# Kernel tuning notes

Measured on AMD Instinct MI355X. Metric: run time of the kernel, lower is better.

## Reference

```python
import jax, jax.numpy as jnp
import numpy as np

D_MODEL = 1024
N_HEADS = 16
HEAD_DIM = D_MODEL // N_HEADS


def setup_inputs() -> dict:
    key = jax.random.key(0)
    k_x, k_qkv, k_out = jax.random.split(key, 3)
    B, T = 4, 2048
    x = jax.random.normal(k_x, (B, T, D_MODEL), dtype=jnp.float32)
    # Linear(bias=False): y = x @ W, with W stored as [in, out]
    W_qkv = jax.random.normal(k_qkv, (D_MODEL, 3 * D_MODEL), dtype=jnp.float32) * (D_MODEL ** -0.5)
    W_out = jax.random.normal(k_out, (D_MODEL, D_MODEL), dtype=jnp.float32) * (D_MODEL ** -0.5)
    return {"x": x, "W_qkv": W_qkv, "W_out": W_out}


def reference(x, W_qkv, W_out):
    B, T, C = x.shape
    H, Dh = N_HEADS, HEAD_DIM
    scale = 1.0 / jnp.sqrt(jnp.asarray(Dh, dtype=x.dtype))

    qkv = x @ W_qkv  # [B,T,3C]
    q, k, v = jnp.split(qkv, 3, axis=-1)

    def split_heads(t):
        return t.reshape(B, T, H, Dh).transpose(0, 2, 1, 3)  # [B,H,T,Dh]

    q, k, v = split_heads(q), split_heads(k), split_heads(v)

    scores = jnp.einsum('bhqd,bhkd->bhqk', q, k) * scale  # [B,H,T,T]
    causal = jnp.tril(jnp.ones((T, T), dtype=bool))
    scores = jnp.where(causal, scores, jnp.asarray(-jnp.inf, dtype=scores.dtype))
    attn = jax.nn.softmax(scores, axis=-1)
    # dropout p=0.0 -> identity
    out = jnp.einsum('bhqk,bhkd->bhqd', attn, v)  # [B,H,T,Dh]
    out = out.transpose(0, 2, 1, 3).reshape(B, T, C)
    return out @ W_out
```

## Files before the change

### kernel.cpp

```cpp
#include <hip/hip_runtime.h>
#include <stdint.h>

typedef unsigned short u16;
typedef float f32x4 __attribute__((ext_vector_type(4)));
typedef short s16x8 __attribute__((ext_vector_type(8)));

#define SEQ 2048
#define DM 1024
#define NH 16
#define HD 64
#define BATCH 4
#define ROWS (BATCH*SEQ)
#define QTILES (SEQ/64)

__device__ __forceinline__ u16 f32_bf16(float f) {
  union { float f; uint32_t u; } c; c.f = f;
  uint32_t u = c.u;
  return (u16)((u + 0x7fffu + ((u >> 16) & 1u)) >> 16);
}
__device__ __forceinline__ u16 f32_bf16_trunc(float f) {
  union { float f; uint32_t u; } c; c.f = f;
  return (u16)(c.u >> 16);
}

#define GLOAD_LDS16(g, l) __builtin_amdgcn_global_load_lds( \
    (__attribute__((address_space(1))) void*)(g),           \
    (__attribute__((address_space(3))) void*)(l), 16, 0, 0)

__global__ __launch_bounds__(256) void cast_bf16_k(const float* __restrict__ in,
                                                   u16* __restrict__ out, int n4) {
  int i = blockIdx.x * 256 + threadIdx.x;
  if (i >= n4) return;
  float4 v = ((const float4*)in)[i];
  ushort4 o;
  o.x = f32_bf16(v.x); o.y = f32_bf16(v.y); o.z = f32_bf16(v.z); o.w = f32_bf16(v.w);
  ((ushort4*)out)[i] = o;
}

__global__ __launch_bounds__(256) void cast_transpose_k(const float* __restrict__ in,
                                                        u16* __restrict__ out, int R, int C) {
  __shared__ float tile[32][33];
  int c0 = blockIdx.x * 32, r0 = blockIdx.y * 32;
  int t = threadIdx.x;
  int lr = t >> 3, lc = (t & 7) * 4;
  float4 v = *(const float4*)(in + (size_t)(r0 + lr) * C + c0 + lc);
  tile[lr][lc] = v.x; tile[lr][lc + 1] = v.y; tile[lr][lc + 2] = v.z; tile[lr][lc + 3] = v.w;
  __syncthreads();
  ushort4 o;
  o.x = f32_bf16(tile[lc + 0][lr]);
  o.y = f32_bf16(tile[lc + 1][lr]);
  o.z = f32_bf16(tile[lc + 2][lr]);
  o.w = f32_bf16(tile[lc + 3][lr]);
  *(ushort4*)(out + (size_t)(c0 + lr) * R + r0 + lc) = o;
}

#define QSCALE 0.18033688011112042f


__device__ __forceinline__ f32x4 mfma16(s16x8 a, s16x8 b, f32x4 c) {
  return __builtin_amdgcn_mfma_f32_16x16x32_bf16(a, b, c, 0, 0, 0);
}

template<int STG, int ENDVM, int LAST>
__device__ __forceinline__ void tile_step(
    const u16* lAc, const u16* lBc,
    const u16* lAn, const u16* lBn,
    u16* lAs, u16* lBs,
    const u16* gA0, const u16* gA1, const u16* gB0, const u16* gB1,
    int d0, int d1, int aoff, int boff,
    s16x8 (&fa)[4], s16x8 (&fb)[4],
    s16x8 (&na)[4], s16x8 (&nb)[4],
    f32x4 (&acc)[8][4])
{
  __builtin_amdgcn_s_barrier();
  __builtin_amdgcn_sched_barrier(0);
  s16x8 f1[4];
#pragma unroll
  for (int mi = 0; mi < 4; ++mi) f1[mi] = *(const s16x8*)&lAc[aoff + 2048 + mi * 512];
  if (STG) { GLOAD_LDS16(gA0, lAs + d0); GLOAD_LDS16(gA1, lAs + d1); }
  asm volatile("s_waitcnt lgkmcnt(4)" ::: "memory");
  __builtin_amdgcn_sched_barrier(0);
  __builtin_amdgcn_s_setprio(1);
#pragma unroll
  for (int mi = 0; mi < 4; ++mi)
#pragma unroll
    for (int ni = 0; ni < 4; ++ni)
      acc[mi][ni] = mfma16(fa[mi], fb[ni], acc[mi][ni]);
  __builtin_amdgcn_s_setprio(0);
  __builtin_amdgcn_sched_barrier(0);
  if (STG) { GLOAD_LDS16(gB0, lBs + d0); GLOAD_LDS16(gB1, lBs + d1); }
  if (ENDVM == 8)      asm volatile("s_waitcnt vmcnt(8)" ::: "memory");
  else if (ENDVM == 4) asm volatile("s_waitcnt vmcnt(4)" ::: "memory");
  else if (ENDVM == 0) asm volatile("s_waitcnt vmcnt(0)" ::: "memory");
  __builtin_amdgcn_s_barrier();
  __builtin_amdgcn_sched_barrier(0);
  if (!LAST) {
#pragma unroll
    for (int ni = 0; ni < 4; ++ni) nb[ni] = *(const s16x8*)&lBn[boff + ni * 512];
#pragma unroll
    for (int mi = 0; mi < 4; ++mi) na[mi] = *(const s16x8*)&lAn[aoff + mi * 512];
    asm volatile("s_waitcnt lgkmcnt(8)" ::: "memory");
  } else {
    asm volatile("s_waitcnt lgkmcnt(0)" ::: "memory");
  }
  __builtin_amdgcn_sched_barrier(0);
  __builtin_amdgcn_s_setprio(1);
#pragma unroll
  for (int mi = 0; mi < 4; ++mi)
#pragma unroll
    for (int ni = 0; ni < 4; ++ni)
      acc[4 + mi][ni] = mfma16(f1[mi], fb[ni], acc[4 + mi][ni]);
  __builtin_amdgcn_s_setprio(0);
  __builtin_amdgcn_sched_barrier(0);
}

__global__ __launch_bounds__(512, 2) void qkv_gemm(
    const u16* __restrict__ A, const u16* __restrict__ Bt,
    u16* __restrict__ Qo, u16* __restrict__ Ko, u16* __restrict__ Vo)
{
  __shared__ u16 lA[4][8192];
  __shared__ u16 lB[4][8192];
  int t = threadIdx.x;

  int flat = blockIdx.y * 12 + blockIdx.x;
  int swz = (flat & 7) * 48 + (flat >> 3);
  int by = swz / 12, bx = swz - by * 12;
  int m0 = by * 256, n0 = bx * 256;

  int lane = t & 63, w = t >> 6;
  int m16 = lane & 15, quad = lane >> 4;
  int wm = w >> 2, wn = w & 3;

  int r0 = t >> 2;
  int scol = ((t & 3) ^ ((t >> 3) & 3)) * 8;
  const u16* Ag0 = A  + (size_t)(m0 + r0) * DM + scol;
  const u16* Ag1 = A  + (size_t)(m0 + 128 + r0) * DM + scol;
  const u16* Bg0 = Bt + (size_t)(n0 + r0) * DM + scol;
  const u16* Bg1 = Bt + (size_t)(n0 + 128 + r0) * DM + scol;
  int d0 = t * 8, d1 = 4096 + t * 8;

  int ka = (quad ^ ((m16 >> 1) & 3)) * 8;
  int aoff = (wm * 128 + m16) * 32 + ka;
  int boff = (wn * 64 + m16) * 32 + ka;

  f32x4 acc[8][4];
#pragma unroll
  for (int mi = 0; mi < 8; ++mi)
#pragma unroll
    for (int ni = 0; ni < 4; ++ni)
#pragma unroll
      for (int r = 0; r < 4; ++r) acc[mi][ni][r] = 0.f;

#pragma unroll
  for (int kt = 0; kt < 3; ++kt) {
    GLOAD_LDS16(Ag0 + kt * 32, lA[kt] + d0);
    GLOAD_LDS16(Ag1 + kt * 32, lA[kt] + d1);
    GLOAD_LDS16(Bg0 + kt * 32, lB[kt] + d0);
    GLOAD_LDS16(Bg1 + kt * 32, lB[kt] + d1);
  }
  asm volatile("s_waitcnt vmcnt(8)" ::: "memory");
  __builtin_amdgcn_s_barrier();
  __builtin_amdgcn_sched_barrier(0);

  s16x8 fa0[4], fb0[4], fa1[4], fb1[4];
#pragma unroll
  for (int ni = 0; ni < 4; ++ni) fb0[ni] = *(const s16x8*)&lB[0][boff + ni * 512];
#pragma unroll
  for (int mi = 0; mi < 4; ++mi) fa0[mi] = *(const s16x8*)&lA[0][aoff + mi * 512];

  for (int it = 0; it < 14; ++it) {
    int T = 2 * it;
    tile_step<1, 8, 0>(lA[T & 3], lB[T & 3], lA[(T + 1) & 3], lB[(T + 1) & 3],
                       lA[(T + 3) & 3], lB[(T + 3) & 3],
                       Ag0 + (T + 3) * 32, Ag1 + (T + 3) * 32,
                       Bg0 + (T + 3) * 32, Bg1 + (T + 3) * 32,
                       d0, d1, aoff, boff, fa0, fb0, fa1, fb1, acc);
    tile_step<1, 8, 0>(lA[(T + 1) & 3], lB[(T + 1) & 3], lA[(T + 2) & 3], lB[(T + 2) & 3],
                       lA[(T + 4) & 3], lB[(T + 4) & 3],
                       Ag0 + (T + 4) * 32, Ag1 + (T + 4) * 32,
                       Bg0 + (T + 4) * 32, Bg1 + (T + 4) * 32,
                       d0, d1, aoff, boff, fa1, fb1, fa0, fb0, acc);
  }
  tile_step<1, 8, 0>(lA[0], lB[0], lA[1], lB[1], lA[3], lB[3],
                     Ag0 + 31 * 32, Ag1 + 31 * 32, Bg0 + 31 * 32, Bg1 + 31 * 32,
                     d0, d1, aoff, boff, fa0, fb0, fa1, fb1, acc);
  tile_step<0, 4, 0>(lA[1], lB[1], lA[2], lB[2], lA[0], lB[0],
                     Ag0, Ag1, Bg0, Bg1, d0, d1, aoff, boff, fa1, fb1, fa0, fb0, acc);
  tile_step<0, 0, 0>(lA[2], lB[2], lA[3], lB[3], lA[0], lB[0],
                     Ag0, Ag1, Bg0, Bg1, d0, d1, aoff, boff, fa0, fb0, fa1, fb1, acc);
  tile_step<0, -1, 1>(lA[3], lB[3], lA[0], lB[0], lA[0], lB[0],
                      Ag0, Ag1, Bg0, Bg1, d0, d1, aoff, boff, fa1, fb1, fa0, fb0, acc);

#pragma unroll
  for (int mi = 0; mi < 8; ++mi) {
    int gr = m0 + wm * 128 + mi * 16 + quad * 4;
    int b = gr >> 11, tt = gr & 2047;
#pragma unroll
    for (int ni = 0; ni < 4; ++ni) {
      int gc = n0 + wn * 64 + ni * 16 + m16;
      int sec = gc >> 10, rem = gc & 1023, h = rem >> 6, d = rem & 63;
      if (sec == 0) {
#pragma unroll
        for (int r = 0; r < 4; ++r)
          Qo[(((size_t)b * NH + h) * SEQ + tt + r) * HD + d] = f32_bf16(acc[mi][ni][r] * QSCALE);
      } else if (sec == 1) {
#pragma unroll
        for (int r = 0; r < 4; ++r)
          Ko[(((size_t)b * NH + h) * SEQ + tt + r) * HD + d] = f32_bf16(acc[mi][ni][r]);
      } else {
        ushort4 o;
        o.x = f32_bf16(acc[mi][ni][0]); o.y = f32_bf16(acc[mi][ni][1]);
        o.z = f32_bf16(acc[mi][ni][2]); o.w = f32_bf16(acc[mi][ni][3]);
        *(ushort4*)&Vo[(((size_t)b * NH + h) * HD + d) * SEQ + tt] = o;
      }
    }
  }
}

template<int EPI>
__global__ __launch_bounds__(256) void gemm_bt(
    const u16* __restrict__ A, const u16* __restrict__ Bt,
    float* __restrict__ Cf, u16* __restrict__ Qo, u16* __restrict__ Ko, u16* __restrict__ Vo,
    int M, int N, int K)
{
  __shared__ u16 As[128 * 32];
  __shared__ u16 Bs[128 * 32];
  int t = threadIdx.x;
  int m0 = blockIdx.y * 128, n0 = blockIdx.x * 128;

  int srow = t >> 2, scol8 = (t & 3) * 8;
  const u16* Ag0 = A  + (size_t)(m0 + srow) * K + scol8;
  const u16* Ag1 = A  + (size_t)(m0 + 64 + srow) * K + scol8;
  const u16* Bg0 = Bt + (size_t)(n0 + srow) * K + scol8;
  const u16* Bg1 = Bt + (size_t)(n0 + 64 + srow) * K + scol8;
  u16* Al0 = As + t * 8;  u16* Al1 = As + 2048 + t * 8;
  u16* Bl0 = Bs + t * 8;  u16* Bl1 = Bs + 2048 + t * 8;

  int lane = t & 63, w = t >> 6;
  int m16 = lane & 15, quad = lane >> 4;
  int wr = (w >> 1) * 64, wc = (w & 1) * 64;

  f32x4 acc[4][4];
#pragma unroll
  for (int mi = 0; mi < 4; ++mi)
#pragma unroll
    for (int ni = 0; ni < 4; ++ni)
#pragma unroll
      for (int r = 0; r < 4; ++r) acc[mi][ni][r] = 0.f;

  for (int k0 = 0; k0 < K; k0 += 32) {
    __syncthreads();
    GLOAD_LDS16(Ag0 + k0, Al0);
    GLOAD_LDS16(Ag1 + k0, Al1);
    GLOAD_LDS16(Bg0 + k0, Bl0);
    GLOAD_LDS16(Bg1 + k0, Bl1);
    __syncthreads();
    s16x8 af[4], bf[4];
#pragma unroll
    for (int mi = 0; mi < 4; ++mi)
      af[mi] = *(const s16x8*)(As + (wr + mi * 16 + m16) * 32 + quad * 8);
#pragma unroll
    for (int ni = 0; ni < 4; ++ni)
      bf[ni] = *(const s16x8*)(Bs + (wc + ni * 16 + m16) * 32 + quad * 8);
#pragma unroll
    for (int mi = 0; mi < 4; ++mi)
#pragma unroll
      for (int ni = 0; ni < 4; ++ni)
        acc[mi][ni] = __builtin_amdgcn_mfma_f32_16x16x32_bf16(af[mi], bf[ni], acc[mi][ni], 0, 0, 0);
  }

  if (EPI == 0) {
#pragma unroll
    for (int mi = 0; mi < 4; ++mi) {
      int gr = m0 + wr + mi * 16 + quad * 4;
#pragma unroll
      for (int ni = 0; ni < 4; ++ni) {
        int gc = n0 + wc + ni * 16 + m16;
#pragma unroll
        for (int r = 0; r < 4; ++r)
          Cf[(size_t)(gr + r) * N + gc] = acc[mi][ni][r];
      }
    }
  } else {
#pragma unroll
    for (int mi = 0; mi < 4; ++mi) {
      int gr = m0 + wr + mi * 16 + quad * 4;
      int b = gr >> 11, tt = gr & 2047;
#pragma unroll
      for (int ni = 0; ni < 4; ++ni) {
        int gc = n0 + wc + ni * 16 + m16;
        int sec = gc >> 10, rem = gc & 1023, h = rem >> 6, d = rem & 63;
        if (sec == 0) {
#pragma unroll
          for (int r = 0; r < 4; ++r)
            Qo[(((size_t)b * NH + h) * SEQ + tt + r) * HD + d] = f32_bf16(acc[mi][ni][r] * QSCALE);
        } else if (sec == 1) {
#pragma unroll
          for (int r = 0; r < 4; ++r)
            Ko[(((size_t)b * NH + h) * SEQ + tt + r) * HD + d] = f32_bf16(acc[mi][ni][r]);
        } else {
          ushort4 o;
          o.x = f32_bf16(acc[mi][ni][0]); o.y = f32_bf16(acc[mi][ni][1]);
          o.z = f32_bf16(acc[mi][ni][2]); o.w = f32_bf16(acc[mi][ni][3]);
          *(ushort4*)&Vo[(((size_t)b * NH + h) * HD + d) * SEQ + tt] = o;
        }
      }
    }
  }
}

__global__ __launch_bounds__(256) void attn_k(
    const u16* __restrict__ Q, const u16* __restrict__ K,
    const u16* __restrict__ Vt_g,
    u16* __restrict__ O)
{
  __shared__ u16 Ks[64][72];
  __shared__ u16 Vt[64][72];
  __shared__ u16 Ps[4][16][72];
  int bh = blockIdx.y;
  int t = threadIdx.x, w = t >> 6, lane = t & 63;
  int m16 = lane & 15, quad = lane >> 4;
  int b = bh >> 4, h = bh & 15;

  int srow = t >> 2, sc = (t & 3) * 16;
  const u16* Kg0 = K    + ((size_t)bh * SEQ + srow) * HD  + sc;
  const u16* Vg0 = Vt_g + ((size_t)bh * HD  + srow) * SEQ + sc;

  for (int half = 0; half < 2; ++half) {
    int qt = half ? (QTILES - 1 - (int)blockIdx.x) : (int)blockIdx.x;
    int q0 = qt * 64;

    const u16* Qb = Q + ((size_t)bh * SEQ + q0 + w * 16 + m16) * HD + quad * 8;
    s16x8 qf0 = *(const s16x8*)Qb;
    s16x8 qf1 = *(const s16x8*)(Qb + 32);

    f32x4 acco[4];
    float l_part[4];
#pragma unroll
    for (int r = 0; r < 4; ++r) l_part[r] = 0.f;
#pragma unroll
    for (int ni = 0; ni < 4; ++ni)
#pragma unroll
      for (int r = 0; r < 4; ++r) acco[ni][r] = 0.f;

    for (int kt = 0; kt <= qt; ++kt) {
      uint4 kv0 = *(const uint4*)(Kg0 + (size_t)kt * 64 * HD);
      uint4 kv1 = *(const uint4*)(Kg0 + (size_t)kt * 64 * HD + 8);
      uint4 vv0 = *(const uint4*)(Vg0 + kt * 64);
      uint4 vv1 = *(const uint4*)(Vg0 + kt * 64 + 8);
      __syncthreads();
      *(uint4*)&Ks[srow][sc]     = kv0;
      *(uint4*)&Ks[srow][sc + 8] = kv1;
      *(uint4*)&Vt[srow][sc]     = vv0;
      *(uint4*)&Vt[srow][sc + 8] = vv1;
      __syncthreads();

      f32x4 sacc[4];
#pragma unroll
      for (int ni = 0; ni < 4; ++ni)
#pragma unroll
        for (int r = 0; r < 4; ++r) sacc[ni][r] = 0.f;
#pragma unroll
      for (int ni = 0; ni < 4; ++ni) {
        s16x8 kf0 = *(const s16x8*)&Ks[ni * 16 + m16][quad * 8];
        s16x8 kf1 = *(const s16x8*)&Ks[ni * 16 + m16][32 + quad * 8];
        sacc[ni] = __builtin_amdgcn_mfma_f32_16x16x32_bf16(qf0, kf0, sacc[ni], 0, 0, 0);
        sacc[ni] = __builtin_amdgcn_mfma_f32_16x16x32_bf16(qf1, kf1, sacc[ni], 0, 0, 0);
      }
      if (kt == qt) {
#pragma unroll
        for (int ni = 0; ni < 4; ++ni)
#pragma unroll
          for (int r = 0; r < 4; ++r)
            if (ni * 16 + m16 > w * 16 + quad * 4 + r) sacc[ni][r] = -1e30f;
      }

#pragma unroll
      for (int ni = 0; ni < 4; ++ni)
#pragma unroll
        for (int r = 0; r < 4; ++r) {
          float p = __builtin_amdgcn_exp2f(sacc[ni][r]);
          l_part[r] += p;
          Ps[w][quad * 4 + r][ni * 16 + m16] = f32_bf16_trunc(p);
        }

#pragma unroll
      for (int ks = 0; ks < 2; ++ks) {
        s16x8 pf = *(const s16x8*)&Ps[w][m16][ks * 32 + quad * 8];
#pragma unroll
        for (int ni = 0; ni < 4; ++ni) {
          s16x8 vf = *(const s16x8*)&Vt[ni * 16 + m16][ks * 32 + quad * 8];
          acco[ni] = __builtin_amdgcn_mfma_f32_16x16x32_bf16(pf, vf, acco[ni], 0, 0, 0);
        }
      }
    }

    float l[4];
#pragma unroll
    for (int r = 0; r < 4; ++r) l[r] = l_part[r];
#pragma unroll
    for (int off = 1; off < 16; off <<= 1)
#pragma unroll
      for (int r = 0; r < 4; ++r) l[r] += __shfl_xor(l[r], off, 64);

#pragma unroll
    for (int r = 0; r < 4; ++r) {
      float inv = 1.f / l[r];
      int trow = q0 + w * 16 + quad * 4 + r;
      size_t base = ((size_t)(b * SEQ + trow)) * DM + h * HD;
#pragma unroll
      for (int ni = 0; ni < 4; ++ni)
        O[base + ni * 16 + m16] = f32_bf16(acco[ni][r] * inv);
    }
  }
}

extern "C" void kernel_launch(void* const* d_in, const int* in_sizes, int n_in,
                              void* d_out, int out_size, void* d_ws, size_t ws_size,
                              hipStream_t stream) {
  const float* x    = (const float*)d_in[0];
  const float* Wqkv = (const float*)d_in[1];
  const float* Wout = (const float*)d_in[2];
  float* out = (float*)d_out;

  u16* ws = (u16*)d_ws;
  size_t off = 0;
  u16* x_bf   = ws + off; off += (size_t)ROWS * DM;
  u16* wqkv_t = ws + off; off += (size_t)(3 * DM) * DM;
  u16* wout_t = ws + off; off += (size_t)DM * DM;
  u16* Qb     = ws + off; off += (size_t)BATCH * NH * SEQ * HD;
  u16* Kb     = ws + off; off += (size_t)BATCH * NH * SEQ * HD;
  u16* Vb     = ws + off; off += (size_t)BATCH * NH * SEQ * HD;
  u16* AO     = ws + off; off += (size_t)ROWS * DM;

  cast_bf16_k<<<(ROWS * DM / 4 + 255) / 256, 256, 0, stream>>>(x, x_bf, ROWS * DM / 4);
  cast_transpose_k<<<dim3(3 * DM / 32, DM / 32), 256, 0, stream>>>(Wqkv, wqkv_t, DM, 3 * DM);
  cast_transpose_k<<<dim3(DM / 32, DM / 32), 256, 0, stream>>>(Wout, wout_t, DM, DM);
  qkv_gemm<<<dim3(12, 32), 512, 0, stream>>>(x_bf, wqkv_t, Qb, Kb, Vb);
  attn_k<<<dim3(QTILES / 2, BATCH * NH), 256, 0, stream>>>(Qb, Kb, Vb, AO);
  gemm_bt<0><<<dim3(DM / 128, ROWS / 128), 256, 0, stream>>>(
      AO, wout_t, out, nullptr, nullptr, nullptr, ROWS, DM, DM);
}
```

Before: 281.0 us.

## Process 128-row query tiles per attention block with XCD-aware head mapping

Each attention block now covers 128 query rows, with each wave holding two 16-row Q fragments. Every K/V tile loaded into LDS is therefore reused across twice as many queries, which halves K/V global traffic and barriers per query. Block indices are remapped so that the blocks of one batch-head land on the same XCD, to improve L2 reuse. The score MFMA is computed transposed, so P can be written to LDS as vector stores and the row sums need fewer shuffles. The trade-off is half as many blocks (512 instead of 1024), more registers per thread and a larger Ps buffer, which may hurt occupancy and load balance.

```diff
diff --git a/kernel.cpp b/kernel.cpp
--- a/kernel.cpp
+++ b/kernel.cpp
@@ -11,7 +11,6 @@
 #define HD 64
 #define BATCH 4
 #define ROWS (BATCH*SEQ)
-#define QTILES (SEQ/64)
 
 __device__ __forceinline__ u16 f32_bf16(float f) {
   union { float f; uint32_t u; } c; c.f = f;
@@ -316,8 +315,11 @@
 {
   __shared__ u16 Ks[64][72];
   __shared__ u16 Vt[64][72];
-  __shared__ u16 Ps[4][16][72];
-  int bh = blockIdx.y;
+  __shared__ u16 Ps[4][32][72];
+  int flat = blockIdx.y * 8 + blockIdx.x;
+  int xcd = flat & 7, pos = flat >> 3;
+  int bh = xcd * 8 + (pos >> 3);
+  int xb = pos & 7;
   int t = threadIdx.x, w = t >> 6, lane = t & 63;
   int m16 = lane & 15, quad = lane >> 4;
   int b = bh >> 4, h = bh & 15;
@@ -327,23 +329,24 @@
   const u16* Vg0 = Vt_g + ((size_t)bh * HD  + srow) * SEQ + sc;
 
   for (int half = 0; half < 2; ++half) {
-    int qt = half ? (QTILES - 1 - (int)blockIdx.x) : (int)blockIdx.x;
-    int q0 = qt * 64;
-
-    const u16* Qb = Q + ((size_t)bh * SEQ + q0 + w * 16 + m16) * HD + quad * 8;
-    s16x8 qf0 = *(const s16x8*)Qb;
-    s16x8 qf1 = *(const s16x8*)(Qb + 32);
-
-    f32x4 acco[4];
-    float l_part[4];
-#pragma unroll
-    for (int r = 0; r < 4; ++r) l_part[r] = 0.f;
-#pragma unroll
-    for (int ni = 0; ni < 4; ++ni)
-#pragma unroll
-      for (int r = 0; r < 4; ++r) acco[ni][r] = 0.f;
-
-    for (int kt = 0; kt <= qt; ++kt) {
+    int qt = half ? (15 - xb) : xb;
+    int q0 = qt * 128;
+
+    const u16* QbA = Q + ((size_t)bh * SEQ + q0 + w * 32 + m16) * HD + quad * 8;
+    s16x8 qA0 = *(const s16x8*)QbA;
+    s16x8 qA1 = *(const s16x8*)(QbA + 32);
+    s16x8 qB0 = *(const s16x8*)(QbA + 16 * HD);
+    s16x8 qB1 = *(const s16x8*)(QbA + 16 * HD + 32);
+
+    f32x4 accA[4], accB[4];
+    float lA = 0.f, lB = 0.f;
+#pragma unroll
+    for (int ni = 0; ni < 4; ++ni)
+#pragma unroll
+      for (int r = 0; r < 4; ++r) { accA[ni][r] = 0.f; accB[ni][r] = 0.f; }
+
+    int ktmax = 2 * qt + 1;
+    for (int kt = 0; kt <= ktmax; ++kt) {
       uint4 kv0 = *(const uint4*)(Kg0 + (size_t)kt * 64 * HD);
       uint4 kv1 = *(const uint4*)(Kg0 + (size_t)kt * 64 * HD + 8);
       uint4 vv0 = *(const uint4*)(Vg0 + kt * 64);
@@ -355,62 +358,80 @@
       *(uint4*)&Vt[srow][sc + 8] = vv1;
       __syncthreads();
 
-      f32x4 sacc[4];
+      f32x4 sA[4], sB[4];
 #pragma unroll
       for (int ni = 0; ni < 4; ++ni)
 #pragma unroll
-        for (int r = 0; r < 4; ++r) sacc[ni][r] = 0.f;
+        for (int r = 0; r < 4; ++r) { sA[ni][r] = 0.f; sB[ni][r] = 0.f; }
 #pragma unroll
       for (int ni = 0; ni < 4; ++ni) {
         s16x8 kf0 = *(const s16x8*)&Ks[ni * 16 + m16][quad * 8];
         s16x8 kf1 = *(const s16x8*)&Ks[ni * 16 + m16][32 + quad * 8];
-        sacc[ni] = __builtin_amdgcn_mfma_f32_16x16x32_bf16(qf0, kf0, sacc[ni], 0, 0, 0);
-        sacc[ni] = __builtin_amdgcn_mfma_f32_16x16x32_bf16(qf1, kf1, sacc[ni], 0, 0, 0);
-      }
-      if (kt == qt) {
-#pragma unroll
-        for (int ni = 0; ni < 4; ++ni)
-#pragma unroll
-          for (int r = 0; r < 4; ++r)
-            if (ni * 16 + m16 > w * 16 + quad * 4 + r) sacc[ni][r] = -1e30f;
-      }
-
-#pragma unroll
-      for (int ni = 0; ni < 4; ++ni)
+        sA[ni] = mfma16(kf0, qA0, sA[ni]);
+        sA[ni] = mfma16(kf1, qA1, sA[ni]);
+        sB[ni] = mfma16(kf0, qB0, sB[ni]);
+        sB[ni] = mfma16(kf1, qB1, sB[ni]);
+      }
+      if (kt >= 2 * qt) {
+        int qga = q0 + w * 32 + m16;
+#pragma unroll
+        for (int ni = 0; ni < 4; ++ni) {
+          int kb = kt * 64 + ni * 16 + quad * 4;
+#pragma unroll
+          for (int r = 0; r < 4; ++r) {
+            if (kb + r > qga)      sA[ni][r] = -1e30f;
+            if (kb + r > qga + 16) sB[ni][r] = -1e30f;
+          }
+        }
+      }
+
+#pragma unroll
+      for (int ni = 0; ni < 4; ++ni) {
+        ushort4 oA, oB;
 #pragma unroll
         for (int r = 0; r < 4; ++r) {
-          float p = __builtin_amdgcn_exp2f(sacc[ni][r]);
-          l_part[r] += p;
-          Ps[w][quad * 4 + r][ni * 16 + m16] = f32_bf16_trunc(p);
+          float pA = __builtin_amdgcn_exp2f(sA[ni][r]);
+          float pB = __builtin_amdgcn_exp2f(sB[ni][r]);
+          lA += pA; lB += pB;
+          ((u16*)&oA)[r] = f32_bf16_trunc(pA);
+          ((u16*)&oB)[r] = f32_bf16_trunc(pB);
         }
+        *(ushort4*)&Ps[w][m16][ni * 16 + quad * 4]      = oA;
+        *(ushort4*)&Ps[w][16 + m16][ni * 16 + quad * 4] = oB;
+      }
 
 #pragma unroll
       for (int ks = 0; ks < 2; ++ks) {
-        s16x8 pf = *(const s16x8*)&Ps[w][m16][ks * 32 + quad * 8];
+        s16x8 pA = *(const s16x8*)&Ps[w][m16][ks * 32 + quad * 8];
+        s16x8 pB = *(const s16x8*)&Ps[w][16 + m16][ks * 32 + quad * 8];
 #pragma unroll
         for (int ni = 0; ni < 4; ++ni) {
           s16x8 vf = *(const s16x8*)&Vt[ni * 16 + m16][ks * 32 + quad * 8];
-          acco[ni] = __builtin_amdgcn_mfma_f32_16x16x32_bf16(pf, vf, acco[ni], 0, 0, 0);
+          accA[ni] = mfma16(pA, vf, accA[ni]);
+          accB[ni] = mfma16(pB, vf, accB[ni]);
         }
       }
     }
 
-    float l[4];
-#pragma unroll
-    for (int r = 0; r < 4; ++r) l[r] = l_part[r];
-#pragma unroll
-    for (int off = 1; off < 16; off <<= 1)
-#pragma unroll
-      for (int r = 0; r < 4; ++r) l[r] += __shfl_xor(l[r], off, 64);
+    lA += __shfl_xor(lA, 16, 64);
+    lA += __shfl_xor(lA, 32, 64);
+    lB += __shfl_xor(lB, 16, 64);
+    lB += __shfl_xor(lB, 32, 64);
 
 #pragma unroll
     for (int r = 0; r < 4; ++r) {
-      float inv = 1.f / l[r];
-      int trow = q0 + w * 16 + quad * 4 + r;
-      size_t base = ((size_t)(b * SEQ + trow)) * DM + h * HD;
-#pragma unroll
-      for (int ni = 0; ni < 4; ++ni)
-        O[base + ni * 16 + m16] = f32_bf16(acco[ni][r] * inv);
+      int src = (lane & 48) | (quad * 4 + r);
+      float la = __shfl(lA, src, 64);
+      float lb = __shfl(lB, src, 64);
+      float ia = 1.f / la, ib = 1.f / lb;
+      int qa = q0 + w * 32 + quad * 4 + r;
+      size_t baseA = ((size_t)(b * SEQ + qa)) * DM + h * HD;
+      size_t baseB = baseA + (size_t)16 * DM;
+#pragma unroll
+      for (int ni = 0; ni < 4; ++ni) {
+        O[baseA + ni * 16 + m16] = f32_bf16(accA[ni][r] * ia);
+        O[baseB + ni * 16 + m16] = f32_bf16(accB[ni][r] * ib);
+      }
     }
   }
 }
@@ -437,7 +458,7 @@
   cast_transpose_k<<<dim3(3 * DM / 32, DM / 32), 256, 0, stream>>>(Wqkv, wqkv_t, DM, 3 * DM);
   cast_transpose_k<<<dim3(DM / 32, DM / 32), 256, 0, stream>>>(Wout, wout_t, DM, DM);
   qkv_gemm<<<dim3(12, 32), 512, 0, stream>>>(x_bf, wqkv_t, Qb, Kb, Vb);
-  attn_k<<<dim3(QTILES / 2, BATCH * NH), 256, 0, stream>>>(Qb, Kb, Vb, AO);
+  attn_k<<<dim3(8, BATCH * NH), 256, 0, stream>>>(Qb, Kb, Vb, AO);
   gemm_bt<0><<<dim3(DM / 128, ROWS / 128), 256, 0, stream>>>(
       AO, wout_t, out, nullptr, nullptr, nullptr, ROWS, DM, DM);
 }
```

Measured after the change: 259.6 us. -7.6%, faster.
